# Performance work log

Measured on AMD Instinct MI355X. Metric: run time of the kernel, lower is better.

Reference implementation:

```python
import jax, jax.numpy as jnp
import numpy as np

N = 100000      # nodes
E = 1600000     # edges (before self-loops)
DIN = 256
D = 128         # dmid == dout
L = 4           # n_layers
ALPHA = 0.5
THETA = 1.0
EPS = 1e-5      # pyg LayerNorm default eps


def setup_inputs() -> dict:
    key = jax.random.key(0)
    ks = jax.random.split(key, 6)
    x = jax.random.normal(ks[0], (N, DIN), jnp.float32)
    edge_index = jax.random.randint(ks[1], (2, E), 0, N)
    lin1_w = jax.random.normal(ks[2], (D, DIN), jnp.float32) * (1.0 / np.sqrt(DIN))
    lin1_b = jnp.zeros((D,), jnp.float32)
    w1 = jax.random.normal(ks[3], (L, D, D), jnp.float32) * (1.0 / np.sqrt(D))
    w2 = jax.random.normal(ks[4], (L, D, D), jnp.float32) * (1.0 / np.sqrt(D))
    norm_w = jnp.ones((D,), jnp.float32)
    norm_b = jnp.zeros((D,), jnp.float32)
    return {"x": x, "edge_index": edge_index, "lin1_w": lin1_w, "lin1_b": lin1_b,
            "w1": w1, "w2": w2, "norm_w": norm_w, "norm_b": norm_b}


def reference(x, edge_index, lin1_w, lin1_b, w1, w2, norm_w, norm_b):
    # --- gcn_norm: add self-loops, symmetric degree normalization ---
    sl = jnp.arange(N)
    row = jnp.concatenate([edge_index[0], sl])  # sources
    col = jnp.concatenate([edge_index[1], sl])  # targets (aggregation index)
    deg = jax.ops.segment_sum(jnp.ones(row.shape[0], jnp.float32), col, num_segments=N)
    dis = jax.lax.rsqrt(deg)  # deg >= 1 thanks to self-loops
    enorm = dis[row] * dis[col]  # [E+N]

    # --- f_0 = relu(lin1(x)); prev_h = 0 so x_0 arg == f_0 ---
    f0 = jax.nn.relu(x @ lin1_w.T + lin1_b)  # [N, D]
    x0 = ALPHA * f0
    f = f0

    for i in range(L):
        beta = float(np.log(THETA / (i + 1) + 1.0))
        # sparse neighbor aggregation: h = A_hat @ f
        h = jax.ops.segment_sum(f[row] * enorm[:, None], col, num_segments=N)
        h = h * (1.0 - ALPHA)
        # shared_weights=False: two separate identity/weight mixes
        out = ((1.0 - beta) * h + beta * (h @ w1[i])
               + (1.0 - beta) * x0 + beta * (x0 @ w2[i]))
        # pyg LayerNorm mode='graph', batch=None: normalize over all nodes+channels
        m = out.mean()
        s = jnp.sqrt(jnp.mean((out - m) ** 2))
        out = (out - m) / (s + EPS) * norm_w + norm_b
        f = jax.nn.relu(out)

    # dmid == dout -> lin2 is Identity
    return jax.nn.relu(f)
```

## Files before the change

### kernel.cpp

```cpp
#include <hip/hip_runtime.h>
#include <math.h>

constexpr int N    = 100000;
constexpr int E    = 1600000;
constexpr int DIN  = 256;
constexpr int D    = 128;
constexpr int L    = 4;
constexpr float EPS = 1e-5f;
constexpr int NBIN = 256;
constexpr int BINW = 391;
constexpr int SLOT = 8192;

constexpr int F0B   = 782;
constexpr int CBB   = 782;
constexpr int PREPB = 64;

typedef __attribute__((ext_vector_type(8))) short bf16x8;
typedef __attribute__((ext_vector_type(4))) float f32x4;
typedef __attribute__((ext_vector_type(2))) float f32x2;

__device__ inline ushort f2b(float f) {
    uint u = __float_as_uint(f);
    uint r = u + 0x7fffu + ((u >> 16) & 1u);
    return (ushort)(r >> 16);
}
__device__ inline float b2f(ushort b) { return __uint_as_float(((uint)b) << 16); }


__global__ __launch_bounds__(512, 2) void k_f0_countbin(
        const float* __restrict__ x, const float* __restrict__ lin1_w,
        const float* __restrict__ bias, ushort* __restrict__ f_bf,
        ushort* __restrict__ x0_bf,
        const int* __restrict__ row, const int* __restrict__ col,
        int* __restrict__ cnt, int* __restrict__ bfill, int2* __restrict__ stag,
        const float* __restrict__ w1, const float* __restrict__ w2, float4 betas,
        ushort* __restrict__ wbc) {
    __shared__ uint4 Bl[4096];
    int t = threadIdx.x;

    if (blockIdx.x >= F0B + CBB) {
        int base = (blockIdx.x - (F0B + CBB)) * 2048 + t * 4;
        #pragma unroll
        for (int j = 0; j < 4; j++) {
            int i = base + j;
            if (i < L * D * 256) {
                int l = i >> 15, r = i & 32767, d = r >> 8, k = r & 255;
                float beta = (l == 0) ? betas.x : (l == 1) ? betas.y
                           : (l == 2) ? betas.z : betas.w;
                float v;
                if (k < 128) v = beta * w1[l * 16384 + k * 128 + d] + ((k == d) ? (1.f - beta) : 0.f);
                else { int kk = k - 128; v = beta * w2[l * 16384 + kk * 128 + d] + ((kk == d) ? (1.f - beta) : 0.f); }
                wbc[l * 32768 + d * 256 + k] = f2b(v);
            }
        }
        return;
    }

    int role = blockIdx.x & 1, rid = blockIdx.x >> 1;

    if (role == 1) {
        int* hist = (int*)Bl;
        int* base = hist + NBIN;
        if (t < NBIN) hist[t] = 0;
        __syncthreads();
        int e0 = rid * 2048 + t * 4;
        bool val = (e0 < E);
        int r[4], c[4], li[4];
        if (val) {
            *(int4*)&c[0] = *(const int4*)(col + e0);
            *(int4*)&r[0] = *(const int4*)(row + e0);
            #pragma unroll
            for (int j = 0; j < 4; j++) {
                atomicAdd(&cnt[c[j]], 1);
                li[j] = atomicAdd(&hist[c[j] / BINW], 1);
            }
        }
        __syncthreads();
        if (t < NBIN) base[t] = hist[t] ? atomicAdd(&bfill[t], hist[t]) : 0;
        __syncthreads();
        if (val) {
            #pragma unroll
            for (int j = 0; j < 4; j++) {
                int b = c[j] / BINW;
                stag[(size_t)b * SLOT + base[b] + li[j]] = make_int2(r[j], c[j]);
            }
        }
        return;
    }

    #pragma unroll
    for (int it = 0; it < 8; it++) {
        int d = it * 512 + t, c = d >> 5, ck = d & 31;
        const float4* src = (const float4*)(lin1_w + c * 256 + ck * 8);
        float4 lo = src[0], hi = src[1];
        uint4 p;
        p.x = (uint)f2b(lo.x) | ((uint)f2b(lo.y) << 16);
        p.y = (uint)f2b(lo.z) | ((uint)f2b(lo.w) << 16);
        p.z = (uint)f2b(hi.x) | ((uint)f2b(hi.y) << 16);
        p.w = (uint)f2b(hi.z) | ((uint)f2b(hi.w) << 16);
        Bl[c * 32 + (ck ^ (c & 7))] = p;
    }
    __syncthreads();

    int wv = t >> 6, lane = t & 63;
    int l16 = lane & 15, g16 = lane >> 4;
    int row0 = (rid * 8 + wv) * 16;
    if (row0 >= N) return;

    const uint4* xb = (const uint4*)(x + (size_t)(row0 + l16) * 256);
    uint4 xr[16];
    #pragma unroll
    for (int ks = 0; ks < 8; ks++) {
        xr[2 * ks]     = xb[ks * 8 + g16 * 2];
        xr[2 * ks + 1] = xb[ks * 8 + g16 * 2 + 1];
    }

    f32x4 acc[8];
    #pragma unroll
    for (int n = 0; n < 8; n++) acc[n] = f32x4{0.f, 0.f, 0.f, 0.f};

    #pragma unroll
    for (int ks = 0; ks < 8; ks++) {
        float4 lo = *(const float4*)&xr[2 * ks];
        float4 hi = *(const float4*)&xr[2 * ks + 1];
        uint4 p;
        p.x = (uint)f2b(lo.x) | ((uint)f2b(lo.y) << 16);
        p.y = (uint)f2b(lo.z) | ((uint)f2b(lo.w) << 16);
        p.z = (uint)f2b(hi.x) | ((uint)f2b(hi.y) << 16);
        p.w = (uint)f2b(hi.z) | ((uint)f2b(hi.w) << 16);
        bf16x8 a = *(bf16x8*)&p;
        int xo = (ks * 4 + g16) ^ (l16 & 7);
        const char* bp = (const char*)Bl + l16 * 512 + xo * 16;
        #pragma unroll
        for (int n = 0; n < 8; n++) {
            bf16x8 b = *(const bf16x8*)(bp + n * 8192);
            acc[n] = __builtin_amdgcn_mfma_f32_16x16x32_bf16(a, b, acc[n], 0, 0, 0);
        }
    }

    float bc[8];
    #pragma unroll
    for (int n = 0; n < 8; n++) bc[n] = bias[n * 16 + l16];
    #pragma unroll
    for (int j = 0; j < 4; j++) {
        int gr = row0 + g16 * 4 + j;
        #pragma unroll
        for (int n = 0; n < 8; n++) {
            float r = fmaxf(acc[n][j] + bc[n], 0.f);
            size_t o = (size_t)gr * 128 + n * 16 + l16;
            f_bf[o] = f2b(r);
            x0_bf[o] = f2b(0.5f * r);
        }
    }
}


__global__ void k_sumdis(const int* __restrict__ cnt, int* __restrict__ bsum,
                         float* __restrict__ dis) {
    __shared__ int s[256];
    int base = blockIdx.x * 1024;
    int t = threadIdx.x;
    int a = 0;
    for (int j = 0; j < 4; j++) {
        int idx = base + t * 4 + j;
        if (idx < N) {
            int cv = cnt[idx];
            a += cv;
            dis[idx] = rsqrtf((float)cv + 1.0f);
        }
    }
    s[t] = a; __syncthreads();
    for (int off = 128; off > 0; off >>= 1) {
        if (t < off) s[t] += s[t + off];
        __syncthreads();
    }
    if (t == 0) bsum[blockIdx.x] = s[0];
}

__global__ void k_scan(int* __restrict__ bsum, int nb) {
    __shared__ int s[128];
    int t = threadIdx.x;
    int v = (t < nb) ? bsum[t] : 0;
    s[t] = v; __syncthreads();
    for (int off = 1; off < 128; off <<= 1) {
        int x = (t >= off) ? s[t - off] : 0;
        __syncthreads();
        s[t] += x;
        __syncthreads();
    }
    if (t < nb) bsum[t] = s[t] - v;
}

__global__ void k_offsets(const int* __restrict__ cnt, const int* __restrict__ bsum,
                          int* __restrict__ offs, int* __restrict__ cur) {
    __shared__ int ls[256];
    int b = blockIdx.x, t = threadIdx.x;
    int base = b * 1024;
    int v[4]; int s = 0;
    for (int j = 0; j < 4; j++) {
        int idx = base + t * 4 + j;
        v[j] = (idx < N) ? cnt[idx] : 0;
        s += v[j];
    }
    ls[t] = s; __syncthreads();
    for (int off = 1; off < 256; off <<= 1) {
        int x = (t >= off) ? ls[t - off] : 0;
        __syncthreads();
        ls[t] += x;
        __syncthreads();
    }
    int excl = ((t == 0) ? 0 : ls[t - 1]) + bsum[b];
    for (int j = 0; j < 4; j++) {
        int idx = base + t * 4 + j;
        if (idx < N) { offs[idx] = excl; cur[idx] = excl; }
        excl += v[j];
        if (idx == N - 1) offs[N] = excl;
    }
}

__global__ __launch_bounds__(256) void k_unbin(const int2* __restrict__ stag,
        const int* __restrict__ bfill, const float* __restrict__ dis,
        int* __restrict__ cur, int2* __restrict__ csr) {
    int b = blockIdx.x & (NBIN - 1);
    int part = blockIdx.x >> 8;
    int n = bfill[b];
    const int2* sbase = stag + (size_t)b * SLOT;
    for (int i = part * 256 + threadIdx.x; i < n; i += 1024) {
        int2 rc = sbase[i];
        float v = dis[rc.x] * dis[rc.y];
        int pos = atomicAdd(&cur[rc.y], 1);
        csr[pos] = make_int2(rc.x, __float_as_int(v));
    }
}


__global__ __launch_bounds__(512, 2) void k_combine_mfma(const ushort* __restrict__ g_bf,
        const ushort* __restrict__ x0_bf, const ushort* __restrict__ wb,
        ushort* __restrict__ h_bf, float* __restrict__ sr) {
    __shared__ uint4 Bl[4096];
    __shared__ float red1[512];
    __shared__ float red2[512];
    int t = threadIdx.x;
    #pragma unroll
    for (int it = 0; it < 8; it++) {
        int d = it * 512 + t, c = d >> 5, ck = d & 31;
        Bl[c * 32 + (ck ^ (c & 7))] = ((const uint4*)wb)[d];
    }
    __syncthreads();

    int wv = t >> 6, lane = t & 63;
    int l16 = lane & 15, g16 = lane >> 4;
    int row0 = (blockIdx.x * 8 + wv) * 16;
    bool active = row0 < N;

    f32x4 acc[8];
    #pragma unroll
    for (int n = 0; n < 8; n++) acc[n] = f32x4{0.f, 0.f, 0.f, 0.f};

    if (active) {
        const uint4* ga = (const uint4*)(g_bf  + (size_t)(row0 + l16) * 128);
        const uint4* xa = (const uint4*)(x0_bf + (size_t)(row0 + l16) * 128);
        uint4 ar[8];
        #pragma unroll
        for (int ks = 0; ks < 4; ks++) ar[ks]     = ga[ks * 4 + g16];
        #pragma unroll
        for (int ks = 0; ks < 4; ks++) ar[ks + 4] = xa[ks * 4 + g16];

        #pragma unroll
        for (int ks = 0; ks < 8; ks++) {
            bf16x8 a = *(bf16x8*)&ar[ks];
            int xo = (ks * 4 + g16) ^ (l16 & 7);
            const char* bp = (const char*)Bl + l16 * 512 + xo * 16;
            #pragma unroll
            for (int n = 0; n < 8; n++) {
                bf16x8 b = *(const bf16x8*)(bp + n * 8192);
                acc[n] = __builtin_amdgcn_mfma_f32_16x16x32_bf16(a, b, acc[n], 0, 0, 0);
            }
        }
    }

    float sum = 0.f, sq = 0.f;
    if (active) {
        #pragma unroll
        for (int n = 0; n < 8; n++)
            #pragma unroll
            for (int j = 0; j < 4; j++) { float v = acc[n][j]; sum += v; sq += v * v; }
        #pragma unroll
        for (int j = 0; j < 4; j++) {
            int gr = row0 + g16 * 4 + j;
            #pragma unroll
            for (int n = 0; n < 8; n++)
                h_bf[(size_t)gr * 128 + n * 16 + l16] = f2b(acc[n][j]);
        }
    }

    red1[t] = sum; red2[t] = sq; __syncthreads();
    for (int off = 256; off > 0; off >>= 1) {
        if (t < off) { red1[t] += red1[t + off]; red2[t] += red2[t + off]; }
        __syncthreads();
    }
    if (t == 0) { atomicAdd(&sr[0], red1[0]); atomicAdd(&sr[1], red2[0]); }
}


template <int AFFINE>
__global__ __launch_bounds__(256) void k_agg(const ushort* __restrict__ src,
        const int* __restrict__ offs, const int2* __restrict__ csr,
        const float* __restrict__ dis, const float* __restrict__ sr,
        const float* __restrict__ nw, const float* __restrict__ nb,
        ushort* __restrict__ g_bf) {
    int node = blockIdx.x * 4 + (threadIdx.x >> 6);
    if (node >= N) return;
    int lane = threadIdx.x & 63;
    int q = lane >> 4, cl = lane & 15;
    const uint4* fu = (const uint4*)src;

    f32x2 sc[4], sh[4];
    if constexpr (AFFINE) {
        const float inv_n = 1.0f / ((float)N * (float)D);
        float m = sr[0] * inv_n;
        float var = fmaxf(sr[1] * inv_n - m * m, 0.f);
        float inv = 1.0f / (sqrtf(var) + EPS);
        #pragma unroll
        for (int p = 0; p < 4; p++) {
            float w0 = nw[cl * 8 + 2 * p], w1 = nw[cl * 8 + 2 * p + 1];
            sc[p] = f32x2{inv * w0, inv * w1};
            sh[p] = f32x2{nb[cl * 8 + 2 * p]     - m * inv * w0,
                          nb[cl * 8 + 2 * p + 1] - m * inv * w1};
        }
    }

    f32x2 a2[4];
    #pragma unroll
    for (int p = 0; p < 4; p++) a2[p] = f32x2{0.f, 0.f};

    auto acc8 = [&](float val, uint4 rv) {
        uint uu[4] = {rv.x, rv.y, rv.z, rv.w};
        f32x2 v2 = {val, val};
        #pragma unroll
        for (int p = 0; p < 4; p++) {
            f32x2 c;
            c.x = __uint_as_float(uu[p] << 16);
            c.y = __uint_as_float(uu[p] & 0xffff0000u);
            if constexpr (AFFINE) {
                c = __builtin_elementwise_fma(c, sc[p], sh[p]);
                c = __builtin_elementwise_max(c, f32x2{0.f, 0.f});
            }
            a2[p] = __builtin_elementwise_fma(v2, c, a2[p]);
        }
    };

    float dv = dis[node];
    acc8((q == 0) ? dv * dv : 0.f, fu[(size_t)node * 16 + cl]);

    int end = offs[node + 1];
    int i = offs[node] + q * 4;
    if (i < end) {
        int2 rA[4], rB[4];
        uint4 wA[4];
        #pragma unroll
        for (int s = 0; s < 4; s++) rA[s] = csr[min(i + s, end - 1)];
        #pragma unroll
        for (int s = 0; s < 4; s++) wA[s] = fu[(size_t)rA[s].x * 16 + cl];
        #pragma unroll
        for (int s = 0; s < 4; s++) rB[s] = csr[min(i + 16 + s, end - 1)];
        while (i + 16 < end) {
            uint4 wB[4];
            #pragma unroll
            for (int s = 0; s < 4; s++) wB[s] = fu[(size_t)rB[s].x * 16 + cl];
            int2 rC[4];
            #pragma unroll
            for (int s = 0; s < 4; s++) rC[s] = csr[min(i + 32 + s, end - 1)];
            #pragma unroll
            for (int s = 0; s < 4; s++) acc8(__int_as_float(rA[s].y), wA[s]);
            #pragma unroll
            for (int s = 0; s < 4; s++) { rA[s] = rB[s]; wA[s] = wB[s]; rB[s] = rC[s]; }
            i += 16;
        }
        #pragma unroll
        for (int s = 0; s < 4; s++) {
            float v = (i + s < end) ? __int_as_float(rA[s].y) : 0.f;
            acc8(v, wA[s]);
        }
    }

    #pragma unroll
    for (int p = 0; p < 4; p++) {
        a2[p].x += __shfl_xor(a2[p].x, 16, 64);
        a2[p].x += __shfl_xor(a2[p].x, 32, 64);
        a2[p].y += __shfl_xor(a2[p].y, 16, 64);
        a2[p].y += __shfl_xor(a2[p].y, 32, 64);
    }
    if (q == 0) {
        uint4 o;
        o.x = (uint)f2b(0.5f * a2[0].x) | ((uint)f2b(0.5f * a2[0].y) << 16);
        o.y = (uint)f2b(0.5f * a2[1].x) | ((uint)f2b(0.5f * a2[1].y) << 16);
        o.z = (uint)f2b(0.5f * a2[2].x) | ((uint)f2b(0.5f * a2[2].y) << 16);
        o.w = (uint)f2b(0.5f * a2[3].x) | ((uint)f2b(0.5f * a2[3].y) << 16);
        ((uint4*)g_bf)[(size_t)node * 16 + cl] = o;
    }
}


__global__ void k_ln_final(const ushort* __restrict__ ob, const float* __restrict__ sr,
                           const float* __restrict__ nw, const float* __restrict__ nb,
                           float* __restrict__ fout) {
    int i = blockIdx.x * 256 + threadIdx.x;
    if (i >= N * 16) return;
    const float inv_n = 1.0f / ((float)N * (float)D);
    float m = sr[0] * inv_n;
    float var = fmaxf(sr[1] * inv_n - m * m, 0.f);
    float inv = 1.0f / (sqrtf(var) + EPS);
    uint4 v = ((const uint4*)ob)[i];
    int c = (i & 15) * 8;
    uint vv[4] = {v.x, v.y, v.z, v.w};
    float r[8];
    #pragma unroll
    for (int qd = 0; qd < 4; qd++) {
        float lo = b2f((ushort)(vv[qd] & 0xffff));
        float hi = b2f((ushort)(vv[qd] >> 16));
        r[2 * qd]     = fmaxf((lo - m) * inv * nw[c + 2 * qd]     + nb[c + 2 * qd], 0.f);
        r[2 * qd + 1] = fmaxf((hi - m) * inv * nw[c + 2 * qd + 1] + nb[c + 2 * qd + 1], 0.f);
    }
    float4 o0 = {r[0], r[1], r[2], r[3]};
    float4 o1 = {r[4], r[5], r[6], r[7]};
    ((float4*)fout)[2 * i] = o0;
    ((float4*)fout)[2 * i + 1] = o1;
}


extern "C" void kernel_launch(void* const* d_in, const int* in_sizes, int n_in,
                              void* d_out, int out_size, void* d_ws, size_t ws_size,
                              hipStream_t stream) {
    const float* x      = (const float*)d_in[0];
    const int*   ei     = (const int*)d_in[1];
    const float* lin1_w = (const float*)d_in[2];
    const float* lin1_b = (const float*)d_in[3];
    const float* w1     = (const float*)d_in[4];
    const float* w2     = (const float*)d_in[5];
    const float* nw     = (const float*)d_in[6];
    const float* nb     = (const float*)d_in[7];
    const int* row = ei;
    const int* col = ei + E;
    float* fout = (float*)d_out;

    char* ws = (char*)d_ws;
    size_t off0 = 0;
    auto alloc = [&](size_t bytes) -> char* {
        char* p = ws + off0;
        off0 = (off0 + bytes + 255) & ~(size_t)255;
        return p;
    };
    ushort* f_bf    = (ushort*)alloc((size_t)N * D * 2);
    ushort* x0_bf   = (ushort*)alloc((size_t)N * D * 2);
    ushort* g_bf    = (ushort*)alloc((size_t)N * D * 2);
    ushort* h_bf    = (ushort*)alloc((size_t)N * D * 2);
    float*  dis     = (float*) alloc((size_t)N * 4);
    char*   zblk    = alloc((size_t)N * 4 + NBIN * 4 + 64);
    int*    cnt     = (int*)zblk;
    int*    bfill   = (int*)(zblk + (size_t)N * 4);
    float*  stats   = (float*)(zblk + (size_t)N * 4 + NBIN * 4);
    int*    offs    = (int*)   alloc((size_t)(N + 1) * 4);
    int*    cur     = (int*)   alloc((size_t)N * 4);
    int*    bsum    = (int*)   alloc((size_t)128 * 4);
    int2*   stag    = (int2*)  alloc((size_t)NBIN * SLOT * 8);
    int2*   csr     = (int2*)  alloc((size_t)E * 8);
    ushort* wbc     = (ushort*)alloc((size_t)L * D * 256 * 2);

    hipMemsetAsync(zblk, 0, (size_t)N * 4 + NBIN * 4 + 64, stream);

    float4 betas;
    betas.x = logf(1.0f / 1.0f + 1.0f);
    betas.y = logf(1.0f / 2.0f + 1.0f);
    betas.z = logf(1.0f / 3.0f + 1.0f);
    betas.w = logf(1.0f / 4.0f + 1.0f);

    k_f0_countbin<<<F0B + CBB + PREPB, 512, 0, stream>>>(
        x, lin1_w, lin1_b, f_bf, x0_bf, row, col, cnt, bfill, stag,
        w1, w2, betas, wbc);

    int nbk = (N + 1023) / 1024;
    k_sumdis<<<nbk, 256, 0, stream>>>(cnt, bsum, dis);
    k_scan<<<1, 128, 0, stream>>>(bsum, nbk);
    k_offsets<<<nbk, 256, 0, stream>>>(cnt, bsum, offs, cur);
    k_unbin<<<NBIN * 4, 256, 0, stream>>>(stag, bfill, dis, cur, csr);

    int GB = (N / 16 + 7) / 8;
    int AGB = (N + 3) / 4;
    for (int i = 0; i < L; i++) {
        if (i == 0)
            k_agg<0><<<AGB, 256, 0, stream>>>(f_bf, offs, csr, dis, nullptr, nw, nb, g_bf);
        else
            k_agg<1><<<AGB, 256, 0, stream>>>(h_bf, offs, csr, dis, stats + 2 * (i - 1),
                                              nw, nb, g_bf);
        k_combine_mfma<<<GB, 512, 0, stream>>>(g_bf, x0_bf, wbc + (size_t)i * D * 256,
                                               h_bf, stats + 2 * i);
    }
    k_ln_final<<<(N * 16 + 255) / 256, 256, 0, stream>>>(h_bf, stats + 6, nw, nb, fout);
}
```

Measured before the change: 529.3 us.

## Replace global degree atomics with per-bin shared-memory counting kernel

Removes the per-edge global atomicAdd on the degree array from the binning pass. Degrees are now counted in a new kernel that walks each staged bin and accumulates into shared memory, so the large degree-array memset is no longer needed. The number of bins drops from 256 to 64 with larger slots, so each bin's node range fits in LDS. The trade-off is an extra launch and a second read of the staged edges. With only 64 blocks the counting kernel may underuse the GPU.

```diff
diff --git a/kernel.cpp b/kernel.cpp
--- a/kernel.cpp
+++ b/kernel.cpp
@@ -7,9 +7,9 @@
 constexpr int D    = 128;
 constexpr int L    = 4;
 constexpr float EPS = 1e-5f;
-constexpr int NBIN = 256;
-constexpr int BINW = 391;
-constexpr int SLOT = 8192;
+constexpr int NBIN = 64;
+constexpr int BINW = 1563;
+constexpr int SLOT = 32768;
 
 constexpr int F0B   = 782;
 constexpr int CBB   = 782;
@@ -32,7 +32,7 @@
         const float* __restrict__ bias, ushort* __restrict__ f_bf,
         ushort* __restrict__ x0_bf,
         const int* __restrict__ row, const int* __restrict__ col,
-        int* __restrict__ cnt, int* __restrict__ bfill, int2* __restrict__ stag,
+        int* __restrict__ bfill, int2* __restrict__ stag,
         const float* __restrict__ w1, const float* __restrict__ w2, float4 betas,
         ushort* __restrict__ wbc) {
     __shared__ uint4 Bl[4096];
@@ -70,10 +70,8 @@
             *(int4*)&c[0] = *(const int4*)(col + e0);
             *(int4*)&r[0] = *(const int4*)(row + e0);
             #pragma unroll
-            for (int j = 0; j < 4; j++) {
-                atomicAdd(&cnt[c[j]], 1);
+            for (int j = 0; j < 4; j++)
                 li[j] = atomicAdd(&hist[c[j] / BINW], 1);
-            }
         }
         __syncthreads();
         if (t < NBIN) base[t] = hist[t] ? atomicAdd(&bfill[t], hist[t]) : 0;
@@ -152,6 +150,23 @@
             x0_bf[o] = f2b(0.5f * r);
         }
     }
+}
+
+
+__global__ __launch_bounds__(256) void k_bincount(const int2* __restrict__ stag,
+        const int* __restrict__ bfill, int* __restrict__ cnt) {
+    __shared__ int lc[BINW];
+    int b = blockIdx.x, t = threadIdx.x;
+    for (int i = t; i < BINW; i += 256) lc[i] = 0;
+    __syncthreads();
+    int n = bfill[b];
+    const int2* sb = stag + (size_t)b * SLOT;
+    for (int i = t; i < n; i += 256)
+        atomicAdd(&lc[sb[i].y - b * BINW], 1);
+    __syncthreads();
+    int n0 = b * BINW;
+    for (int i = t; i < BINW; i += 256)
+        if (n0 + i < N) cnt[n0 + i] = lc[i];
 }
 
 
@@ -222,10 +237,10 @@
         const int* __restrict__ bfill, const float* __restrict__ dis,
         int* __restrict__ cur, int2* __restrict__ csr) {
     int b = blockIdx.x & (NBIN - 1);
-    int part = blockIdx.x >> 8;
+    int part = blockIdx.x >> 6;
     int n = bfill[b];
     const int2* sbase = stag + (size_t)b * SLOT;
-    for (int i = part * 256 + threadIdx.x; i < n; i += 1024) {
+    for (int i = part * 256 + threadIdx.x; i < n; i += 4096) {
         int2 rc = sbase[i];
         float v = dis[rc.x] * dis[rc.y];
         int pos = atomicAdd(&cur[rc.y], 1);
@@ -456,10 +471,10 @@
     ushort* g_bf    = (ushort*)alloc((size_t)N * D * 2);
     ushort* h_bf    = (ushort*)alloc((size_t)N * D * 2);
     float*  dis     = (float*) alloc((size_t)N * 4);
-    char*   zblk    = alloc((size_t)N * 4 + NBIN * 4 + 64);
-    int*    cnt     = (int*)zblk;
-    int*    bfill   = (int*)(zblk + (size_t)N * 4);
-    float*  stats   = (float*)(zblk + (size_t)N * 4 + NBIN * 4);
+    int*    cnt     = (int*)   alloc((size_t)N * 4);
+    char*   zblk    = alloc((size_t)NBIN * 4 + 64);
+    int*    bfill   = (int*)zblk;
+    float*  stats   = (float*)(zblk + NBIN * 4);
     int*    offs    = (int*)   alloc((size_t)(N + 1) * 4);
     int*    cur     = (int*)   alloc((size_t)N * 4);
     int*    bsum    = (int*)   alloc((size_t)128 * 4);
@@ -467,7 +482,7 @@
     int2*   csr     = (int2*)  alloc((size_t)E * 8);
     ushort* wbc     = (ushort*)alloc((size_t)L * D * 256 * 2);
 
-    hipMemsetAsync(zblk, 0, (size_t)N * 4 + NBIN * 4 + 64, stream);
+    hipMemsetAsync(zblk, 0, (size_t)NBIN * 4 + 64, stream);
 
     float4 betas;
     betas.x = logf(1.0f / 1.0f + 1.0f);
@@ -476,14 +491,15 @@
     betas.w = logf(1.0f / 4.0f + 1.0f);
 
     k_f0_countbin<<<F0B + CBB + PREPB, 512, 0, stream>>>(
-        x, lin1_w, lin1_b, f_bf, x0_bf, row, col, cnt, bfill, stag,
+        x, lin1_w, lin1_b, f_bf, x0_bf, row, col, bfill, stag,
         w1, w2, betas, wbc);
 
+    k_bincount<<<NBIN, 256, 0, stream>>>(stag, bfill, cnt);
     int nbk = (N + 1023) / 1024;
     k_sumdis<<<nbk, 256, 0, stream>>>(cnt, bsum, dis);
     k_scan<<<1, 128, 0, stream>>>(bsum, nbk);
     k_offsets<<<nbk, 256, 0, stream>>>(cnt, bsum, offs, cur);
-    k_unbin<<<NBIN * 4, 256, 0, stream>>>(stag, bfill, dis, cur, csr);
+    k_unbin<<<NBIN * 16, 256, 0, stream>>>(stag, bfill, dis, cur, csr);
 
     int GB = (N / 16 + 7) / 8;
     int AGB = (N + 3) / 4;
```

Measured after the change: 556.9 us. +5.2%, slower.
